# Kernel tuning notes

Hardware: AMD Instinct MI355X
Metric: run time of the kernel (lower is better)

The kernel has to match this reference:

```python
import jax, jax.numpy as jnp
import numpy as np
from jax import lax


def log_g(x):
    # log of g(x) = x + 0.5 for x >= 0, sigmoid(x) for x < 0
    return jnp.where(x >= 0, jnp.log(jax.nn.relu(x) + 0.5), -jax.nn.softplus(-x))


def setup_inputs() -> dict:
    key = jax.random.key(0)
    k1, k2, k3, k4 = jax.random.split(key, 4)
    N, L, H_in, H = 8, 4096, 1024, 1024
    x = jax.random.normal(k1, (N, L, H_in), dtype=jnp.float32)
    W = jax.random.normal(k2, (2 * H, H_in), dtype=jnp.float32) * (1.0 / np.sqrt(H_in))
    b = jax.random.normal(k3, (2 * H,), dtype=jnp.float32) * 0.01
    hx = jax.random.uniform(k4, (N, H), dtype=jnp.float32)  # positive initial state
    return {"x": x, "W": W, "b": b, "hx": hx}


def reference(x, W, b, hx):
    # linear_ih: (N, L, 2H)
    zh = jnp.einsum('nli,oi->nlo', x, W) + b
    z, h_inter = jnp.split(zh, 2, axis=-1)  # each (N, L, H)
    log_z = -jax.nn.softplus(-z)            # log sigmoid(z)
    log_coeffs = -jax.nn.softplus(z)        # log (1 - sigmoid(z))
    log_h0 = jnp.log(hx)[:, None, :]        # (N, 1, H)
    log_tilde_h = log_g(h_inter)
    log_values = jnp.concatenate([log_h0, log_z + log_tilde_h], axis=1)  # (N, L+1, H)
    # Heinsen parallel scan in log space
    a_star = jnp.pad(jnp.cumsum(log_coeffs, axis=1), ((0, 0), (1, 0), (0, 0)))  # (N, L+1, H)
    log_h = a_star + lax.cumlogsumexp(log_values - a_star, axis=1)
    h = jnp.exp(log_h)
    return h[:, 1:]  # (N, L, H)
```

## Files before the change

### kernel.cpp

```cpp
#include <hip/hip_runtime.h>
#include <hip/hip_bf16.h>
#include <hip/hip_fp16.h>


#define N_B   8
#define L_SEQ 4096
#define H_DIM 1024
#define K_DIM 1024
#define O_DIM 2048
#define M_TOT (N_B * L_SEQ)

#define BM 128
#define BN 128
#define BK 64

#define NCHUNK 128
#define CLEN   (L_SEQ / NCHUNK)
#define NCH    (N_B * H_DIM)

typedef unsigned short ushort_t;
typedef unsigned short us8 __attribute__((ext_vector_type(8)));
typedef __bf16 v8bf __attribute__((ext_vector_type(8)));
typedef float f32x4 __attribute__((ext_vector_type(4)));

static __device__ __forceinline__ ushort_t f2bf(float f) {
    __hip_bfloat16 h = __float2bfloat16(f);
    return *reinterpret_cast<ushort_t*>(&h);
}

static __device__ __forceinline__ void dma16(const ushort_t* g, ushort_t* l) {
    __builtin_amdgcn_global_load_lds(
        (const __attribute__((address_space(1))) unsigned int*)g,
        (__attribute__((address_space(3))) unsigned int*)l,
        16, 0, 0);
}

__global__ __launch_bounds__(256) void cvt_f32_bf16(
    const float* __restrict__ src, ushort_t* __restrict__ dst)
{
    const int i = blockIdx.x * 256 + threadIdx.x;
    const float4 f0 = ((const float4*)src)[2 * i];
    const float4 f1 = ((const float4*)src)[2 * i + 1];
    us8 o;
    o[0] = f2bf(f0.x); o[1] = f2bf(f0.y); o[2] = f2bf(f0.z); o[3] = f2bf(f0.w);
    o[4] = f2bf(f1.x); o[5] = f2bf(f1.y); o[6] = f2bf(f1.z); o[7] = f2bf(f1.w);
    ((us8*)dst)[i] = o;
}

__global__ __launch_bounds__(256) void cvt_w_perm(
    const float* __restrict__ src, ushort_t* __restrict__ dst)
{
    const int i  = blockIdx.x * 256 + threadIdx.x;
    const int op = i >> 7;
    const int k  = (i & 127) * 8;
    const int B  = op >> 4, t = op & 15;
    const int orig = (B & 1) * 1024 + (B >> 1) * 16 + t;
    const float4* s = (const float4*)(src + (size_t)orig * K_DIM + k);
    const float4 f0 = s[0], f1 = s[1];
    us8 o;
    o[0] = f2bf(f0.x); o[1] = f2bf(f0.y); o[2] = f2bf(f0.z); o[3] = f2bf(f0.w);
    o[4] = f2bf(f1.x); o[5] = f2bf(f1.y); o[6] = f2bf(f1.z); o[7] = f2bf(f1.w);
    *(us8*)(dst + (size_t)op * K_DIM + k) = o;
}

__global__ __launch_bounds__(256) void bias_perm(
    const float* __restrict__ b, float* __restrict__ bp)
{
    const int i = blockIdx.x * 256 + threadIdx.x;
    const int B = i >> 4, t = i & 15;
    bp[i] = b[(B & 1) * 1024 + (B >> 1) * 16 + t];
}

__device__ __forceinline__ void gate_av(float z, float hi, float& a, float& v)
{
    const float e  = __expf(-z);
    const float sz = 1.0f / (1.0f + e);
    a = e * sz;
    const float g = (hi >= 0.0f) ? (hi + 0.5f)
                                 : (1.0f / (1.0f + __expf(-hi)));
    v = sz * g;
}

__global__ __launch_bounds__(256) void gemm_zh(
    const ushort_t* __restrict__ Xb,
    const ushort_t* __restrict__ Wb,
    const float* __restrict__ biasp,
    __half2* __restrict__ avbuf,
    float* __restrict__ Aar,
    float* __restrict__ Bar)
{
    __shared__ ushort_t As[BM * BK];
    __shared__ ushort_t Bs[BN * BK];

    const int tid    = threadIdx.x;
    const int wave   = tid >> 6;
    const int lane   = tid & 63;
    const int lane15 = lane & 15;
    const int quad   = lane >> 4;

    const int n0 = blockIdx.x * BN;
    const int m0 = blockIdx.y * BM;

    const int lrow = lane >> 3;
    const int jj   = (lane & 7) ^ lrow;
    const ushort_t* gA = Xb + (size_t)(m0 + wave * 8 + lrow) * K_DIM + jj * 8;
    const ushort_t* gB = Wb + (size_t)(n0 + wave * 8 + lrow) * K_DIM + jj * 8;
    ushort_t* lA = &As[(wave * 8) * BK];
    ushort_t* lB = &Bs[(wave * 8) * BK];

    const int wm = (wave >> 1) * 64;
    const int wn = (wave & 1) * 64;

    int offA[2][4], offB[2][4];
#pragma unroll
    for (int s = 0; s < 2; ++s) {
#pragma unroll
        for (int t = 0; t < 4; ++t) {
            const int rowA = wm + t * 16 + lane15;
            offA[s][t] = rowA * BK + (((s * 4 + quad) ^ (rowA & 7)) * 8);
            const int rowB = wn + t * 16 + lane15;
            offB[s][t] = rowB * BK + (((s * 4 + quad) ^ (rowB & 7)) * 8);
        }
    }

    const f32x4 fzero = {0.f, 0.f, 0.f, 0.f};
    f32x4 acc[4][4];
#pragma unroll
    for (int i = 0; i < 4; ++i)
#pragma unroll
        for (int j = 0; j < 4; ++j)
            acc[i][j] = fzero;

    for (int kt = 0; kt < K_DIM / BK; ++kt) {
        __syncthreads();
#pragma unroll
        for (int r = 0; r < 4; ++r) {
            dma16(gA + (size_t)r * 32 * K_DIM + kt * BK, lA + r * 32 * BK);
            dma16(gB + (size_t)r * 32 * K_DIM + kt * BK, lB + r * 32 * BK);
        }
        __syncthreads();

#pragma unroll
        for (int s = 0; s < 2; ++s) {
            v8bf af[4], bfr[4];
#pragma unroll
            for (int t = 0; t < 4; ++t) af[t]  = *(const v8bf*)(&As[offA[s][t]]);
#pragma unroll
            for (int t = 0; t < 4; ++t) bfr[t] = *(const v8bf*)(&Bs[offB[s][t]]);
#pragma unroll
            for (int i = 0; i < 4; ++i)
#pragma unroll
                for (int j = 0; j < 4; ++j)
                    acc[i][j] = __builtin_amdgcn_mfma_f32_16x16x32_bf16(
                        af[i], bfr[j], acc[i][j], 0, 0, 0);
        }
    }

    float bv[4];
#pragma unroll
    for (int j = 0; j < 4; ++j)
        bv[j] = biasp[n0 + wn + j * 16 + lane15];

    const int chbase = ((n0 + wn) >> 1) + lane15;

    float Ai[4][2], Bi[4][2];

#pragma unroll
    for (int i = 0; i < 4; ++i) {
        float A[2] = {1.f, 1.f};
        float Bc[2] = {0.f, 0.f};
#pragma unroll
        for (int r = 0; r < 4; ++r) {
            const size_t row = (size_t)(m0 + wm + i * 16 + quad * 4 + r);
            __half2* prow = avbuf + row * H_DIM + chbase;
#pragma unroll
            for (int jp = 0; jp < 2; ++jp) {
                const float z  = acc[i][2 * jp][r]     + bv[2 * jp];
                const float hh = acc[i][2 * jp + 1][r] + bv[2 * jp + 1];
                float a, v;
                gate_av(z, hh, a, v);
                const __half2 h2 = __floats2half2_rn(a, v);
                prow[jp * 16] = h2;
                const float2 f = __half22float2(h2);
                Bc[jp] = fmaf(f.x, Bc[jp], f.y);
                A[jp] *= f.x;
            }
        }
#pragma unroll
        for (int jp = 0; jp < 2; ++jp) {
#pragma unroll
            for (int d = 16; d < 64; d <<= 1) {
                const float Ay = __shfl_xor(A[jp],  d);
                const float By = __shfl_xor(Bc[jp], d);
                Bc[jp] = (lane & d) ? fmaf(A[jp], By, Bc[jp])
                                    : fmaf(Ay, Bc[jp], By);
                A[jp] *= Ay;
            }
            Ai[i][jp] = A[jp];
            Bi[i][jp] = Bc[jp];
        }
    }

    if (lane < 16) {
#pragma unroll
        for (int cc = 0; cc < 2; ++cc) {
            const int grow = m0 + wm + cc * 32;
            const int n    = grow >> 12;
            const int cch  = (grow & (L_SEQ - 1)) >> 5;
            const size_t o = (size_t)cch * NCH + (size_t)n * H_DIM + chbase;
#pragma unroll
            for (int jp = 0; jp < 2; ++jp) {
                const float A0 = Ai[2 * cc][jp],     B0 = Bi[2 * cc][jp];
                const float A1 = Ai[2 * cc + 1][jp], B1 = Bi[2 * cc + 1][jp];
                Aar[o + jp * 16] = A1 * A0;
                Bar[o + jp * 16] = fmaf(A1, B0, B1);
            }
        }
    }
}

__global__ __launch_bounds__(256) void scan_phase2(
    const float* __restrict__ Aar, const float* __restrict__ Bar,
    const float* __restrict__ hx, float* __restrict__ seed)
{
    const int ch = blockIdx.x * 256 + threadIdx.x;
    float carry = hx[ch];
#pragma unroll 8
    for (int c = 0; c < NCHUNK; ++c) {
        seed[c * NCH + ch] = carry;
        carry = fmaf(Aar[c * NCH + ch], carry, Bar[c * NCH + ch]);
    }
}

__global__ __launch_bounds__(256) void scan_phase3(
    const __half2* __restrict__ avbuf,
    const float* __restrict__ seed, float* __restrict__ out)
{
    const int idx = blockIdx.x * 256 + threadIdx.x;
    const int h4  = (idx & 255) << 2;
    const int n   = (idx >> 8) & 7;
    const int c   = idx >> 11;
    const size_t base = ((size_t)(n * L_SEQ + c * CLEN)) * H_DIM + h4;
    const float4* avp = (const float4*)(avbuf + base);
    float* op = out + base;

    const size_t so = (size_t)c * NCH + n * H_DIM + h4;
    float h0[4];
    *(f32x4*)h0 = *(const f32x4*)(seed + so);

#pragma unroll 8
    for (int s = 0; s < CLEN; ++s) {
        float4 avr = avp[(size_t)s * (H_DIM / 4)];
        const __half2* a2 = (const __half2*)&avr;
#pragma unroll
        for (int j = 0; j < 4; ++j) {
            const float2 av = __half22float2(a2[j]);
            h0[j] = fmaf(av.x, h0[j], av.y);
        }
        f32x4 hv = *(const f32x4*)h0;
        __builtin_nontemporal_store(hv, (f32x4*)(op + (size_t)s * H_DIM));
    }
}

extern "C" void kernel_launch(void* const* d_in, const int* in_sizes, int n_in,
                              void* d_out, int out_size, void* d_ws, size_t ws_size,
                              hipStream_t stream)
{
    const float* X    = (const float*)d_in[0];
    const float* Wm   = (const float*)d_in[1];
    const float* bias = (const float*)d_in[2];
    const float* hx   = (const float*)d_in[3];
    float* out = (float*)d_out;

    char* ws = (char*)d_ws;
    ushort_t* wb   = (ushort_t*)ws;
    __half2*  avbuf = (__half2*)(ws + (size_t)O_DIM * K_DIM * 2);
    float*    seed = (float*)((char*)avbuf + (size_t)M_TOT * H_DIM * 4);
    float*    biasp = seed + (size_t)NCHUNK * NCH;

    ushort_t* xb = (ushort_t*)d_out;
    float* Aar = out + (size_t)M_TOT * H_DIM / 2;
    float* Bar = Aar + (size_t)NCHUNK * NCH;

    cvt_w_perm<<<O_DIM * K_DIM / 8 / 256, 256, 0, stream>>>(Wm, wb);
    bias_perm<<<O_DIM / 256, 256, 0, stream>>>(bias, biasp);
    cvt_f32_bf16<<<M_TOT * K_DIM / 8 / 256, 256, 0, stream>>>(X, xb);

    dim3 ggrid(O_DIM / BN, M_TOT / BM);
    gemm_zh<<<ggrid, 256, 0, stream>>>(xb, wb, biasp, avbuf, Aar, Bar);

    scan_phase2<<<NCH / 256, 256, 0, stream>>>(Aar, Bar, hx, seed);

    const int p3_blocks = (NCH / 4) * NCHUNK / 256;
    scan_phase3<<<p3_blocks, 256, 0, stream>>>(avbuf, seed, out);
}
```

Baseline: 443.5 us.

## Fuse scan into GEMM epilogue with decoupled look-back across tiles

The separate chunk-carry and chunk-replay scan kernels are replaced by a single GEMM kernel whose epilogue computes the linear recurrence in place. Tiles are handed out in order through an atomic ticket. Each tile publishes its aggregate (A,B) and then its inclusive state, and later tiles look back through earlier tiles along the sequence using flags, in the style of a decoupled look-back scan. This removes the fp16 a/v intermediate buffer and its write and re-read, plus two kernel launches. The cost is serialisation through spin-waits and strided scalar output stores from the MFMA layout.

Result: slower. 1.526 ms (+244.2%).

```diff
diff --git a/kernel.cpp b/kernel.cpp
--- a/kernel.cpp
+++ b/kernel.cpp
@@ -13,10 +13,10 @@
 #define BM 128
 #define BN 128
 #define BK 64
-
-#define NCHUNK 128
-#define CLEN   (L_SEQ / NCHUNK)
-#define NCH    (N_B * H_DIM)
+#define TILES_M (M_TOT / BM)
+#define TILES_N (O_DIM / BN)
+#define NTILES  (TILES_M * TILES_N)
+#define MT_PER_BATCH (L_SEQ / BM)
 
 typedef unsigned short ushort_t;
 typedef unsigned short us8 __attribute__((ext_vector_type(8)));
@@ -33,6 +33,19 @@
         (const __attribute__((address_space(1))) unsigned int*)g,
         (__attribute__((address_space(3))) unsigned int*)l,
         16, 0, 0);
+}
+
+static __device__ __forceinline__ float ald(const float* p) {
+    return __hip_atomic_load(p, __ATOMIC_RELAXED, __HIP_MEMORY_SCOPE_AGENT);
+}
+static __device__ __forceinline__ void ast(float* p, float v) {
+    __hip_atomic_store(p, v, __ATOMIC_RELAXED, __HIP_MEMORY_SCOPE_AGENT);
+}
+
+__global__ __launch_bounds__(256) void init_sync(int* __restrict__ flags)
+{
+    const int i = blockIdx.x * 256 + threadIdx.x;
+    if (i <= NTILES * 2) flags[i] = 0;
 }
 
 __global__ __launch_bounds__(256) void cvt_f32_bf16(
@@ -81,16 +94,18 @@
     v = sz * g;
 }
 
-__global__ __launch_bounds__(256) void gemm_zh(
+__global__ __launch_bounds__(256) void gemm_scan(
     const ushort_t* __restrict__ Xb,
     const ushort_t* __restrict__ Wb,
     const float* __restrict__ biasp,
-    __half2* __restrict__ avbuf,
-    float* __restrict__ Aar,
-    float* __restrict__ Bar)
+    const float* __restrict__ hx,
+    float* __restrict__ out,
+    float* __restrict__ st,
+    int* __restrict__ flags)
 {
     __shared__ ushort_t As[BM * BK];
     __shared__ ushort_t Bs[BN * BK];
+    __shared__ int s_id;
 
     const int tid    = threadIdx.x;
     const int wave   = tid >> 6;
@@ -98,8 +113,11 @@
     const int lane15 = lane & 15;
     const int quad   = lane >> 4;
 
-    const int n0 = blockIdx.x * BN;
-    const int m0 = blockIdx.y * BM;
+    if (tid == 0) s_id = atomicAdd(flags + NTILES * 2, 1);
+    __syncthreads();
+    const int id = s_id;
+    const int m0 = (id >> 4) * BM;
+    const int n0 = (id & 15) * BN;
 
     const int lrow = lane >> 3;
     const int jj   = (lane & 7) ^ lrow;
@@ -161,104 +179,173 @@
     for (int j = 0; j < 4; ++j)
         bv[j] = biasp[n0 + wn + j * 16 + lane15];
 
-    const int chbase = ((n0 + wn) >> 1) + lane15;
-
-    float Ai[4][2], Bi[4][2];
-
-#pragma unroll
-    for (int i = 0; i < 4; ++i) {
-        float A[2] = {1.f, 1.f};
-        float Bc[2] = {0.f, 0.f};
-#pragma unroll
-        for (int r = 0; r < 4; ++r) {
-            const size_t row = (size_t)(m0 + wm + i * 16 + quad * 4 + r);
-            __half2* prow = avbuf + row * H_DIM + chbase;
+    __half2 av[4][4][2];
+#pragma unroll
+    for (int i = 0; i < 4; ++i)
+#pragma unroll
+        for (int r = 0; r < 4; ++r)
 #pragma unroll
             for (int jp = 0; jp < 2; ++jp) {
                 const float z  = acc[i][2 * jp][r]     + bv[2 * jp];
                 const float hh = acc[i][2 * jp + 1][r] + bv[2 * jp + 1];
                 float a, v;
                 gate_av(z, hh, a, v);
-                const __half2 h2 = __floats2half2_rn(a, v);
-                prow[jp * 16] = h2;
-                const float2 f = __half22float2(h2);
-                Bc[jp] = fmaf(f.x, Bc[jp], f.y);
-                A[jp] *= f.x;
-            }
-        }
+                av[i][r][jp] = __floats2half2_rn(a, v);
+            }
+
+    float Aw[2] = {1.f, 1.f}, Bw[2] = {0.f, 0.f};
+    float Aex[4][2], Bex[4][2];
+#pragma unroll
+    for (int i = 0; i < 4; ++i) {
 #pragma unroll
         for (int jp = 0; jp < 2; ++jp) {
-#pragma unroll
-            for (int d = 16; d < 64; d <<= 1) {
-                const float Ay = __shfl_xor(A[jp],  d);
-                const float By = __shfl_xor(Bc[jp], d);
-                Bc[jp] = (lane & d) ? fmaf(A[jp], By, Bc[jp])
-                                    : fmaf(Ay, Bc[jp], By);
-                A[jp] *= Ay;
-            }
-            Ai[i][jp] = A[jp];
-            Bi[i][jp] = Bc[jp];
-        }
-    }
-
-    if (lane < 16) {
-#pragma unroll
-        for (int cc = 0; cc < 2; ++cc) {
-            const int grow = m0 + wm + cc * 32;
-            const int n    = grow >> 12;
-            const int cch  = (grow & (L_SEQ - 1)) >> 5;
-            const size_t o = (size_t)cch * NCH + (size_t)n * H_DIM + chbase;
+            float Ar = 1.f, Br = 0.f;
+#pragma unroll
+            for (int r = 0; r < 4; ++r) {
+                const float2 f = __half22float2(av[i][r][jp]);
+                Br = fmaf(f.x, Br, f.y); Ar *= f.x;
+            }
+            float Au = __shfl_up(Ar, 16), Bu = __shfl_up(Br, 16);
+            if (quad >= 1) { Br = fmaf(Ar, Bu, Br); Ar *= Au; }
+            Au = __shfl_up(Ar, 32); Bu = __shfl_up(Br, 32);
+            if (quad >= 2) { Br = fmaf(Ar, Bu, Br); Ar *= Au; }
+            float Ax = __shfl_up(Ar, 16), Bx = __shfl_up(Br, 16);
+            if (quad == 0) { Ax = 1.f; Bx = 0.f; }
+            Aex[i][jp] = Ax * Aw[jp];
+            Bex[i][jp] = fmaf(Ax, Bw[jp], Bx);
+            const float Af = __shfl(Ar, 48 + lane15);
+            const float Bf = __shfl(Br, 48 + lane15);
+            Bw[jp] = fmaf(Af, Bw[jp], Bf); Aw[jp] *= Af;
+        }
+    }
+
+    float* ldsf = (float*)As;
+    const int wn2 = wn >> 6;
+    const int sl0 = wn2 * 32 + lane15;
+    __syncthreads();
+
+    if (wm == 0 && lane < 16) {
+#pragma unroll
+        for (int jp = 0; jp < 2; ++jp) {
+            ldsf[sl0 + jp * 16]      = Aw[jp];
+            ldsf[64 + sl0 + jp * 16] = Bw[jp];
+        }
+    }
+    __syncthreads();
+
+    float hws[2];
+    if (wm) {
+        float A0[2], B0[2], hin[2];
+#pragma unroll
+        for (int jp = 0; jp < 2; ++jp) {
+            A0[jp] = ldsf[sl0 + jp * 16];
+            B0[jp] = ldsf[64 + sl0 + jp * 16];
+        }
+        float Ab[2], Bb[2];
+#pragma unroll
+        for (int jp = 0; jp < 2; ++jp) {
+            Ab[jp] = Aw[jp] * A0[jp];
+            Bb[jp] = fmaf(Aw[jp], B0[jp], Bw[jp]);
+        }
+        const int  mtile  = id >> 4;
+        const bool bstart = (mtile & (MT_PER_BATCH - 1)) == 0;
+        const size_t sb   = (size_t)id * 192;
+        const int  fidx   = id * 2 + wn2;
+
+        if (!bstart) {
+            if (lane < 16) {
+#pragma unroll
+                for (int jp = 0; jp < 2; ++jp) {
+                    ast(st + sb + sl0 + jp * 16, Ab[jp]);
+                    ast(st + sb + 64 + sl0 + jp * 16, Bb[jp]);
+                }
+            }
+            __threadfence();
+            if (lane == 0)
+                __hip_atomic_store(flags + fidx, 1, __ATOMIC_RELEASE,
+                                   __HIP_MEMORY_SCOPE_AGENT);
+        }
+
+        if (bstart) {
+#pragma unroll
+            for (int jp = 0; jp < 2; ++jp)
+                hin[jp] = hx[(size_t)(m0 >> 12) * H_DIM +
+                             ((n0 + wn) >> 1) + lane15 + jp * 16];
+        } else {
+            float MA[2] = {1.f, 1.f}, MB[2] = {0.f, 0.f};
+            int j = id - TILES_N;
+            for (;;) {
+                int f;
+                do {
+                    f = __hip_atomic_load(flags + j * 2 + wn2, __ATOMIC_ACQUIRE,
+                                          __HIP_MEMORY_SCOPE_AGENT);
+                    f = __builtin_amdgcn_readfirstlane(f);
+                    if (!f) __builtin_amdgcn_s_sleep(2);
+                } while (!f);
+                const size_t jb = (size_t)j * 192;
+                if (f == 2) {
+#pragma unroll
+                    for (int jp = 0; jp < 2; ++jp) {
+                        const float hp = ald(st + jb + 128 + sl0 + jp * 16);
+                        hin[jp] = fmaf(MA[jp], hp, MB[jp]);
+                    }
+                    break;
+                }
+#pragma unroll
+                for (int jp = 0; jp < 2; ++jp) {
+                    const float Aj = ald(st + jb + sl0 + jp * 16);
+                    const float Bj = ald(st + jb + 64 + sl0 + jp * 16);
+                    MB[jp] = fmaf(MA[jp], Bj, MB[jp]); MA[jp] *= Aj;
+                }
+                j -= TILES_N;
+            }
+        }
+
+        if (lane < 16) {
+#pragma unroll
+            for (int jp = 0; jp < 2; ++jp)
+                ast(st + sb + 128 + sl0 + jp * 16,
+                    fmaf(Ab[jp], hin[jp], Bb[jp]));
+        }
+        __threadfence();
+        if (lane == 0)
+            __hip_atomic_store(flags + fidx, 2, __ATOMIC_RELEASE,
+                               __HIP_MEMORY_SCOPE_AGENT);
+
+        if (lane < 16) {
+#pragma unroll
+            for (int jp = 0; jp < 2; ++jp)
+                ldsf[128 + sl0 + jp * 16] = hin[jp];
+        }
+#pragma unroll
+        for (int jp = 0; jp < 2; ++jp)
+            hws[jp] = fmaf(A0[jp], hin[jp], B0[jp]);
+    }
+    __syncthreads();
+    if (!wm) {
+#pragma unroll
+        for (int jp = 0; jp < 2; ++jp)
+            hws[jp] = ldsf[128 + sl0 + jp * 16];
+    }
+
+    const int cw = (n0 + wn) >> 1;
+#pragma unroll
+    for (int i = 0; i < 4; ++i) {
+        float h0[2];
+#pragma unroll
+        for (int jp = 0; jp < 2; ++jp)
+            h0[jp] = fmaf(Aex[i][jp], hws[jp], Bex[i][jp]);
+#pragma unroll
+        for (int r = 0; r < 4; ++r) {
+            const int row = m0 + wm + i * 16 + quad * 4 + r;
+            float* po = out + (size_t)row * H_DIM + cw + lane15;
 #pragma unroll
             for (int jp = 0; jp < 2; ++jp) {
-                const float A0 = Ai[2 * cc][jp],     B0 = Bi[2 * cc][jp];
-                const float A1 = Ai[2 * cc + 1][jp], B1 = Bi[2 * cc + 1][jp];
-                Aar[o + jp * 16] = A1 * A0;
-                Bar[o + jp * 16] = fmaf(A1, B0, B1);
-            }
-        }
-    }
-}
-
-__global__ __launch_bounds__(256) void scan_phase2(
-    const float* __restrict__ Aar, const float* __restrict__ Bar,
-    const float* __restrict__ hx, float* __restrict__ seed)
-{
-    const int ch = blockIdx.x * 256 + threadIdx.x;
-    float carry = hx[ch];
-#pragma unroll 8
-    for (int c = 0; c < NCHUNK; ++c) {
-        seed[c * NCH + ch] = carry;
-        carry = fmaf(Aar[c * NCH + ch], carry, Bar[c * NCH + ch]);
-    }
-}
-
-__global__ __launch_bounds__(256) void scan_phase3(
-    const __half2* __restrict__ avbuf,
-    const float* __restrict__ seed, float* __restrict__ out)
-{
-    const int idx = blockIdx.x * 256 + threadIdx.x;
-    const int h4  = (idx & 255) << 2;
-    const int n   = (idx >> 8) & 7;
-    const int c   = idx >> 11;
-    const size_t base = ((size_t)(n * L_SEQ + c * CLEN)) * H_DIM + h4;
-    const float4* avp = (const float4*)(avbuf + base);
-    float* op = out + base;
-
-    const size_t so = (size_t)c * NCH + n * H_DIM + h4;
-    float h0[4];
-    *(f32x4*)h0 = *(const f32x4*)(seed + so);
-
-#pragma unroll 8
-    for (int s = 0; s < CLEN; ++s) {
-        float4 avr = avp[(size_t)s * (H_DIM / 4)];
-        const __half2* a2 = (const __half2*)&avr;
-#pragma unroll
-        for (int j = 0; j < 4; ++j) {
-            const float2 av = __half22float2(a2[j]);
-            h0[j] = fmaf(av.x, h0[j], av.y);
-        }
-        f32x4 hv = *(const f32x4*)h0;
-        __builtin_nontemporal_store(hv, (f32x4*)(op + (size_t)s * H_DIM));
+                const float2 f = __half22float2(av[i][r][jp]);
+                h0[jp] = fmaf(f.x, h0[jp], f.y);
+                __builtin_nontemporal_store(h0[jp], po + jp * 16);
+            }
+        }
     }
 }
 
@@ -273,24 +360,16 @@
     float* out = (float*)d_out;
 
     char* ws = (char*)d_ws;
-    ushort_t* wb   = (ushort_t*)ws;
-    __half2*  avbuf = (__half2*)(ws + (size_t)O_DIM * K_DIM * 2);
-    float*    seed = (float*)((char*)avbuf + (size_t)M_TOT * H_DIM * 4);
-    float*    biasp = seed + (size_t)NCHUNK * NCH;
-
-    ushort_t* xb = (ushort_t*)d_out;
-    float* Aar = out + (size_t)M_TOT * H_DIM / 2;
-    float* Bar = Aar + (size_t)NCHUNK * NCH;
-
+    ushort_t* wb    = (ushort_t*)ws;
+    ushort_t* xb    = (ushort_t*)(ws + (size_t)O_DIM * K_DIM * 2);
+    float*    biasp = (float*)(ws + (size_t)(4 + 64) * 1024 * 1024);
+    float*    st    = biasp + 64 * 1024 / 4;
+    int*      flags = (int*)(st + (size_t)NTILES * 192);
+
+    init_sync<<<(NTILES * 2 + 256) / 256 + 1, 256, 0, stream>>>(flags);
     cvt_w_perm<<<O_DIM * K_DIM / 8 / 256, 256, 0, stream>>>(Wm, wb);
     bias_perm<<<O_DIM / 256, 256, 0, stream>>>(bias, biasp);
     cvt_f32_bf16<<<M_TOT * K_DIM / 8 / 256, 256, 0, stream>>>(X, xb);
 
-    dim3 ggrid(O_DIM / BN, M_TOT / BM);
-    gemm_zh<<<ggrid, 256, 0, stream>>>(xb, wb, biasp, avbuf, Aar, Bar);
-
-    scan_phase2<<<NCH / 256, 256, 0, stream>>>(Aar, Bar, hx, seed);
-
-    const int p3_blocks = (NCH / 4) * NCHUNK / 256;
-    scan_phase3<<<p3_blocks, 256, 0, stream>>>(avbuf, seed, out);
-}
+    gemm_scan<<<NTILES, 256, 0, stream>>>(xb, wb, biasp, hx, out, st, flags);
+}
```
